# Performance work log

Measured on AMD Instinct MI355X. Metric: run time of the kernel, lower is better.

The kernel has to match this reference:

```python
import jax, jax.numpy as jnp
import numpy as np

SCALES = [2 ** i for i in range(11)]  # init: scales=10 -> [1,2,...,1024]
B, N, C, K = 8, 1024, 256, 4096


def setup_inputs() -> dict:
    key = jax.random.key(0)
    k1, k2, k3 = jax.random.split(key, 3)
    f_BNC = jax.random.normal(k1, (B, N, C), dtype=jnp.float32)
    base = jax.random.normal(k2, (K, C), dtype=jnp.float32)          # orthogonal-init codebook base
    proj_w = jax.random.normal(k3, (C, C), dtype=jnp.float32) / np.float32(np.sqrt(C))  # xavier-ish
    proj_b = jnp.zeros((C,), dtype=jnp.float32)
    return {"f_BNC": f_BNC, "base": base, "proj_w": proj_w, "proj_b": proj_b}


def _linear_interp(x, out_size):
    # x: [B, C, n] -> [B, C, out_size], matches F.interpolate(mode='linear', align_corners=False)
    n = x.shape[-1]
    scale = n / out_size
    src = jnp.maximum((jnp.arange(out_size, dtype=jnp.float32) + 0.5) * scale - 0.5, 0.0)
    i0 = jnp.floor(src).astype(jnp.int32)
    i1 = jnp.minimum(i0 + 1, n - 1)
    w = (src - i0.astype(jnp.float32)).astype(x.dtype)
    return x[..., i0] * (1.0 - w) + x[..., i1] * w


def reference(f_BNC, base, proj_w, proj_b):
    sg = jax.lax.stop_gradient
    # update_embedding(): embedding = proj(base)
    embedding = base @ proj_w.T + proj_b                 # [K, C]
    emb_ng = sg(embedding)
    e_sq = jnp.sum(emb_ng * emb_ng, axis=1)              # [K]

    f_BCN = jnp.transpose(f_BNC, (0, 2, 1))              # [B, C, N]
    f_ng = sg(f_BCN)
    f_rest = f_ng
    f_hat = jnp.zeros_like(f_ng)
    commit = jnp.float32(0.0)
    qlat = jnp.float32(0.0)
    SN = len(SCALES)

    for pn in SCALES:
        # area interpolation == exact mean pooling since N % pn == 0
        rest_BCp = f_rest.reshape(B, C, pn, N // pn).mean(axis=-1)       # [B, C, pn]
        q = jnp.transpose(rest_BCp, (0, 2, 1)).reshape(-1, C)            # [B*pn, C]
        # squared-distance to codebook (gradients never flow through d: argmin only)
        d = jnp.sum(q * q, axis=1, keepdims=True) + e_sq - 2.0 * (q @ emb_ng.T)  # [B*pn, K]
        idx = jnp.argmin(d, axis=1)                                      # [B*pn]
        h_BnC = embedding[idx].reshape(B, pn, C)                         # gather (grad flows to codebook)
        h_BCn = _linear_interp(jnp.transpose(h_BnC, (0, 2, 1)), N)       # [B, C, N]
        f_hat = f_hat + h_BCn
        # residual feeds only argmin at the next scale -> dead gradient path in torch too
        f_rest = f_rest - sg(h_BCn)
        commit = commit + 0.25 * jnp.mean((sg(f_hat) - f_BCN) ** 2)
        qlat = qlat + jnp.mean((f_hat - f_ng) ** 2)

    commit = commit / SN
    qlat = qlat / SN
    # straight-through: f_hat = (f_hat.data - f_no_grad) + f_BCN
    f_out = sg(f_hat) - f_ng + f_BCN
    return (jnp.transpose(f_out, (0, 2, 1)), commit, qlat)
```

## Files before the change

### kernel.cpp

```cpp
#include <hip/hip_runtime.h>
#include <cfloat>

#define BB 8
#define NN 1024
#define CC 256
#define KK 4096
#define SN 11
#define BNC (BB*NN*CC)
#define RMAX 8192

typedef __attribute__((ext_vector_type(8))) _Float16 half8;
typedef __attribute__((ext_vector_type(4))) float f32x4;

__device__ __forceinline__ void split2(float v, ushort& h, ushort& l) {
    union { _Float16 f; ushort u; } a, b;
    a.f = (_Float16)v;
    b.f = (_Float16)(v - (float)a.f);
    h = a.u; l = b.u;
}

__global__ void transpose_pw(const float* __restrict__ pw, float* __restrict__ pwT) {
    int j = blockIdx.x;
    int c = threadIdx.x;
    pwT[j * CC + c] = pw[c * CC + j];
}

__global__ __launch_bounds__(256) void embed_kernel(
    const float* __restrict__ base, const float* __restrict__ pwT,
    const float* __restrict__ pb, float* __restrict__ emb,
    ushort* __restrict__ eh, ushort* __restrict__ el, float* __restrict__ esq) {
    __shared__ float bs[16][CC];
    __shared__ float wpart[16][4];
    int k0 = blockIdx.x * 16;
    int t = threadIdx.x;
    int w = t >> 6, lane = t & 63;
    for (int i = t; i < 16 * CC; i += 256) bs[i >> 8][i & 255] = base[k0 * CC + i];
    __syncthreads();
    float acc[16];
#pragma unroll
    for (int m = 0; m < 16; ++m) acc[m] = 0.f;
    for (int j = 0; j < CC; ++j) {
        float wv = pwT[j * CC + t];
#pragma unroll
        for (int m = 0; m < 16; ++m) acc[m] += bs[m][j] * wv;
    }
    float bias = pb[t];
#pragma unroll
    for (int m = 0; m < 16; ++m) {
        float v = acc[m] + bias;
        int o = (k0 + m) * CC + t;
        emb[o] = v;
        ushort h, l;
        split2(64.f * v, h, l);
        eh[o] = h; el[o] = l;
        float sq = v * v;
#pragma unroll
        for (int d = 1; d < 64; d <<= 1) sq += __shfl_xor(sq, d);
        if (lane == 0) wpart[m][w] = sq;
    }
    __syncthreads();
    if (t < 16) esq[k0 + t] = wpart[t][0] + wpart[t][1] + wpart[t][2] + wpart[t][3];
}

__global__ __launch_bounds__(256) void init_pool16(const float* __restrict__ f,
                                                   float* __restrict__ p16) {
    int blk = blockIdx.x;
    int t = threadIdx.x;
    size_t base = (size_t)blk * 16 * CC + t;
    float s = 0.f;
#pragma unroll
    for (int j = 0; j < 16; ++j) s += f[base + (size_t)j * CC];
    p16[(size_t)blk * CC + t] = s;
}

__global__ void poolB(const float* __restrict__ p16, float* __restrict__ qf, int pnn) {
    int r = blockIdx.x;
    int b = r / pnn, p = r - b * pnn;
    int g16 = 64 / pnn;
    int c4 = threadIdx.x;
    const float4* src = (const float4*)(p16 + ((size_t)b * 64 + (size_t)p * g16) * CC) + c4;
    float4 s = make_float4(0.f, 0.f, 0.f, 0.f);
    for (int i = 0; i < g16; ++i) {
        float4 v = src[(size_t)i * 64];
        s.x += v.x; s.y += v.y; s.z += v.z; s.w += v.w;
    }
    float inv = 1.f / (float)(g16 * 16);
    s.x *= inv; s.y *= inv; s.z *= inv; s.w *= inv;
    ((float4*)(qf + (size_t)r * CC))[c4] = s;
}

__global__ __launch_bounds__(256, 4) void dist_small(
    const float* __restrict__ qf, const float* __restrict__ emb,
    const float* __restrict__ esq, int R,
    float* __restrict__ pval, int* __restrict__ pidx) {
    __shared__ float qs[32][CC];
    __shared__ float es[64][33];
    int t = threadIdx.x;
    int ws = t >> 6, j = t & 63;
    int k0 = blockIdx.x * 64;
    int r0c = blockIdx.y * 32;
    {
        int row = t >> 3, c0 = (t & 7) * 32;
        int gr = r0c + row;
#pragma unroll
        for (int i = 0; i < 8; ++i) {
            float4 v = (gr < R) ? *(const float4*)&qf[(size_t)gr * CC + c0 + 4 * i]
                                : make_float4(0.f, 0.f, 0.f, 0.f);
            *(float4*)&qs[row][c0 + 4 * i] = v;
        }
    }
    float acc[8];
#pragma unroll
    for (int ri = 0; ri < 8; ++ri) acc[ri] = 0.f;
    for (int ck = 0; ck < 8; ++ck) {
        __syncthreads();
        {
            int code = t >> 2, cb = (t & 3) * 8;
            float4 v0 = *(const float4*)&emb[(size_t)(k0 + code) * CC + ck * 32 + cb];
            float4 v1 = *(const float4*)&emb[(size_t)(k0 + code) * CC + ck * 32 + cb + 4];
            es[code][cb + 0] = v0.x; es[code][cb + 1] = v0.y;
            es[code][cb + 2] = v0.z; es[code][cb + 3] = v0.w;
            es[code][cb + 4] = v1.x; es[code][cb + 5] = v1.y;
            es[code][cb + 6] = v1.z; es[code][cb + 7] = v1.w;
        }
        __syncthreads();
        for (int c = 0; c < 32; ++c) {
            float ev = es[j][c];
#pragma unroll
            for (int ri = 0; ri < 8; ++ri)
                acc[ri] += qs[ws + 4 * ri][ck * 32 + c] * ev;
        }
    }
    float esv = esq[k0 + j];
#pragma unroll
    for (int ri = 0; ri < 8; ++ri) {
        int r = r0c + ws + 4 * ri;
        if (r >= R) continue;
        float v = esv - 2.f * acc[ri];
        int bi = k0 + j;
#pragma unroll
        for (int d = 1; d < 64; d <<= 1) {
            float ov = __shfl_xor(v, d);
            int oi = __shfl_xor(bi, d);
            if (ov < v || (ov == v && oi < bi)) { v = ov; bi = oi; }
        }
        if (j == 0) {
            pval[(size_t)r * 64 + blockIdx.x] = v;
            pidx[(size_t)r * 64 + blockIdx.x] = bi;
        }
    }
}

__global__ __launch_bounds__(256, 2) void dist_mfma(
    const ushort* __restrict__ qh, const ushort* __restrict__ ql,
    const ushort* __restrict__ eh, const ushort* __restrict__ el,
    const float* __restrict__ esq,
    float* __restrict__ pval, int* __restrict__ pidx) {
    __shared__ ushort tiles[4096 * 8];
    __shared__ float wv[2][128];
    __shared__ int wi[2][128];
    int t = threadIdx.x;
    int w = t >> 6, lane = t & 63;
    int l15 = lane & 15, hi = lane >> 4;
    int wr = w >> 1, wc = w & 1;
    int r0 = blockIdx.x * 128;
    int kb = blockIdx.y;
    int k0 = kb * 128;

    f32x4 acc[4][4];
#pragma unroll
    for (int mi = 0; mi < 4; ++mi)
#pragma unroll
        for (int ni = 0; ni < 4; ++ni) acc[mi][ni] = (f32x4){0.f, 0.f, 0.f, 0.f};

    for (int ck = 0; ck < 4; ++ck) {
        __syncthreads();
#pragma unroll
        for (int it = 0; it < 16; ++it) {
            int s = it * 256 + t;
            const ushort* g;
            if (s < 2048) {
                int a = s >> 10;
                int rem = s & 1023;
                int row = rem >> 3, sr = rem & 7;
                int c = (ck << 6) + ((sr ^ (row & 7)) << 3);
                g = (a ? ql : qh) + (size_t)(r0 + row) * CC + c;
            } else {
                int s2 = s - 2048;
                int b = s2 >> 10;
                int rem = s2 & 1023;
                int kcol = rem >> 3, sr = rem & 7;
                int c = (ck << 6) + ((sr ^ (kcol & 7)) << 3);
                g = (b ? el : eh) + (size_t)(k0 + kcol) * CC + c;
            }
            ushort* lb = &tiles[(size_t)(it * 256 + (w << 6)) * 8];
            __builtin_amdgcn_global_load_lds(
                (const __attribute__((address_space(1))) unsigned int*)g,
                (__attribute__((address_space(3))) unsigned int*)lb, 16, 0, 0);
        }
        __syncthreads();

#pragma unroll
        for (int kk = 0; kk < 2; ++kk) {
            int cs = (kk << 2) + hi;
            half8 bf0[4], bf1[4], af[4];
#pragma unroll
            for (int ni = 0; ni < 4; ++ni) {
                int kcol = (wc << 6) + (ni << 4) + l15;
                int sb = 2048 + (kcol << 3) + (cs ^ (kcol & 7));
                bf0[ni] = *(const half8*)&tiles[sb * 8];
                bf1[ni] = *(const half8*)&tiles[(sb + 1024) * 8];
            }
#pragma unroll
            for (int mi = 0; mi < 4; ++mi) {
                int row = (wr << 6) + (mi << 4) + l15;
                af[mi] = *(const half8*)&tiles[((row << 3) + (cs ^ (row & 7))) * 8];
            }
#pragma unroll
            for (int mi = 0; mi < 4; ++mi)
#pragma unroll
                for (int ni = 0; ni < 4; ++ni)
                    acc[mi][ni] = __builtin_amdgcn_mfma_f32_16x16x32_f16(af[mi], bf0[ni], acc[mi][ni], 0, 0, 0);
#pragma unroll
            for (int mi = 0; mi < 4; ++mi)
#pragma unroll
                for (int ni = 0; ni < 4; ++ni)
                    acc[mi][ni] = __builtin_amdgcn_mfma_f32_16x16x32_f16(af[mi], bf1[ni], acc[mi][ni], 0, 0, 0);
#pragma unroll
            for (int mi = 0; mi < 4; ++mi) {
                int row = (wr << 6) + (mi << 4) + l15;
                af[mi] = *(const half8*)&tiles[(1024 + (row << 3) + (cs ^ (row & 7))) * 8];
            }
#pragma unroll
            for (int mi = 0; mi < 4; ++mi)
#pragma unroll
                for (int ni = 0; ni < 4; ++ni)
                    acc[mi][ni] = __builtin_amdgcn_mfma_f32_16x16x32_f16(af[mi], bf0[ni], acc[mi][ni], 0, 0, 0);
        }
    }

    int cbase = k0 + (wc << 6) + l15;
    float es4[4];
#pragma unroll
    for (int ni = 0; ni < 4; ++ni) es4[ni] = 4096.f * esq[cbase + ni * 16];
#pragma unroll
    for (int mi = 0; mi < 4; ++mi) {
#pragma unroll
        for (int reg = 0; reg < 4; ++reg) {
            float v = es4[0] - 2.f * acc[mi][0][reg];
            int i = cbase;
#pragma unroll
            for (int ni = 1; ni < 4; ++ni) {
                float v1 = es4[ni] - 2.f * acc[mi][ni][reg];
                if (v1 < v) { v = v1; i = cbase + ni * 16; }
            }
#pragma unroll
            for (int d = 1; d < 16; d <<= 1) {
                float ov = __shfl_xor(v, d);
                int oi = __shfl_xor(i, d);
                if (ov < v || (ov == v && oi < i)) { v = ov; i = oi; }
            }
            if (l15 == 0) {
                int row = (wr << 6) + (mi << 4) + (hi << 2) + reg;
                wv[wc][row] = v;
                wi[wc][row] = i;
            }
        }
    }
    __syncthreads();
    if (t < 128) {
        float v = wv[0][t];
        int i = wi[0][t];
        float ov = wv[1][t];
        int oi = wi[1][t];
        if (ov < v || (ov == v && oi < i)) { v = ov; i = oi; }
        pval[(size_t)(r0 + t) * 64 + kb] = v;
        pidx[(size_t)(r0 + t) * 64 + kb] = i;
    }
}

__global__ __launch_bounds__(256) void update_pool(
    const float* __restrict__ emb, const float* __restrict__ pval,
    const int* __restrict__ pidx, const float* __restrict__ f,
    float* __restrict__ fhat, float* __restrict__ parts,
    ushort* __restrict__ qh, ushort* __restrict__ ql,
    float* __restrict__ qf, float* __restrict__ p16u,
    int pn, int gn, int pnn, int ks) {
    int blk = blockIdx.x;
    int b = blk >> 6, n16 = blk & 63;
    int t = threadIdx.x;
    int w = t >> 6, lane = t & 63;
    int n0 = n16 * 16;
    const float scale = (float)pn * (1.0f / 1024.0f);
    float s_lo = (n0 + 0.5f) * scale - 0.5f;
    if (s_lo < 0.f) s_lo = 0.f;
    int r_lo = (int)s_lo;
    float s_hi = (n0 + 15.5f) * scale - 0.5f;
    if (s_hi < 0.f) s_hi = 0.f;
    int r_hi = min((int)s_hi + 1, pn - 1);
    int cnt = r_hi - r_lo + 1;
    __shared__ int sidx[20];
    for (int ri = w; ri < cnt; ri += 4) {
        size_t rowg = (size_t)(b * pn + r_lo + ri) * 64;
        float v = (lane < ks) ? pval[rowg + lane] : FLT_MAX;
        int i = (lane < ks) ? pidx[rowg + lane] : 0x7fffffff;
#pragma unroll
        for (int d = 1; d < 64; d <<= 1) {
            float ov = __shfl_xor(v, d);
            int oi = __shfl_xor(i, d);
            if (ov < v || (ov == v && oi < i)) { v = ov; i = oi; }
        }
        if (lane == 0) sidx[ri] = i;
    }
    __syncthreads();
    float sq = 0.f;
    float pr = 0.f;
    for (int j = 0; j < 16; ++j) {
        int n = n0 + j;
        float s = (n + 0.5f) * scale - 0.5f;
        if (s < 0.f) s = 0.f;
        int i0 = (int)s;
        float wgt = s - (float)i0;
        int i1 = min(i0 + 1, pn - 1);
        int k0 = sidx[i0 - r_lo];
        int k1 = sidx[i1 - r_lo];
        float e0 = emb[(size_t)k0 * CC + t];
        float e1 = emb[(size_t)k1 * CC + t];
        float h = (1.f - wgt) * e0 + wgt * e1;
        size_t o = ((size_t)b * NN + n) * CC + t;
        float fh = fhat[o] + h;
        fhat[o] = fh;
        float fv = f[o];
        float d = fh - fv;
        sq += d * d;
        pr += (fv - fh);
        if (gn > 0 && gn < 16 && ((j & (gn - 1)) == (gn - 1))) {
            float mean = pr * (1.f / (float)gn);
            ushort H, L;
            split2(64.f * mean, H, L);
            size_t r = (size_t)b * pnn + (size_t)(n / gn);
            qh[r * CC + t] = H;
            ql[r * CC + t] = L;
            pr = 0.f;
        }
    }
    if (gn == 16) qf[(size_t)blk * CC + t] = pr * (1.f / 16.f);
    else if (gn >= 32) p16u[(size_t)blk * CC + t] = pr;
    for (int off = 32; off > 0; off >>= 1) sq += __shfl_down(sq, off);
    __shared__ float wred[4];
    if (lane == 0) wred[w] = sq;
    __syncthreads();
    if (t == 0) parts[blk] = wred[0] + wred[1] + wred[2] + wred[3];
}

__global__ void reduce_final(const float* __restrict__ parts, float* __restrict__ out) {
    __shared__ float red[256];
    int t = threadIdx.x;
    float s = 0.f;
    for (int i = t; i < SN * 512; i += 256) s += parts[i];
    red[t] = s;
    __syncthreads();
    for (int k = 128; k > 0; k >>= 1) {
        if (t < k) red[t] += red[t + k];
        __syncthreads();
    }
    if (t == 0) {
        float mean_sum = red[0] / (float)BNC;
        out[BNC] = 0.25f * mean_sum / (float)SN;
        out[BNC + 1] = mean_sum / (float)SN;
    }
}

extern "C" void kernel_launch(void* const* d_in, const int* in_sizes, int n_in,
                              void* d_out, int out_size, void* d_ws, size_t ws_size,
                              hipStream_t stream) {
    const float* f    = (const float*)d_in[0];
    const float* base = (const float*)d_in[1];
    const float* pw   = (const float*)d_in[2];
    const float* pb   = (const float*)d_in[3];
    float* out = (float*)d_out;

    float* emb   = (float*)d_ws;
    float* esq   = emb + (size_t)KK * CC;
    float* pwT   = esq + KK;
    float* parts = pwT + (size_t)CC * CC;
    float* pval  = parts + (size_t)SN * 512;
    float* p16   = pval + (size_t)RMAX * 64;
    float* p16u  = p16 + (size_t)BB * 64 * CC;
    float* qf    = p16u + (size_t)BB * 64 * CC;
    int*   pidx  = (int*)(qf + (size_t)512 * CC);
    ushort* eh = (ushort*)(pidx + (size_t)RMAX * 64);
    ushort* el = eh + (size_t)KK * CC;
    ushort* qh = el + (size_t)KK * CC;
    ushort* ql = qh + (size_t)RMAX * CC;

    hipMemsetAsync(out, 0, (size_t)BNC * sizeof(float), stream);

    transpose_pw<<<CC, CC, 0, stream>>>(pw, pwT);
    embed_kernel<<<KK / 16, 256, 0, stream>>>(base, pwT, pb, emb, eh, el, esq);
    init_pool16<<<BB * 64, 256, 0, stream>>>(f, p16);
    poolB<<<8, 64, 0, stream>>>(p16, qf, 1);

    for (int sidx = 0; sidx < SN; ++sidx) {
        int pn = 1 << sidx;
        int R = BB * pn;
        int ks;
        if (pn <= 64) {
            dim3 grid(64, (R + 31) / 32);
            dist_small<<<grid, 256, 0, stream>>>(qf, emb, esq, R, pval, pidx);
            ks = 64;
        } else {
            dist_mfma<<<dim3(R / 128, 32), 256, 0, stream>>>(qh, ql, eh, el, esq, pval, pidx);
            ks = 32;
        }
        int pnn = (sidx < SN - 1) ? (pn << 1) : 0;
        int gn = pnn ? (NN / pnn) : 0;
        update_pool<<<BB * 64, 256, 0, stream>>>(emb, pval, pidx, f, out,
                                                 parts + (size_t)sidx * 512,
                                                 qh, ql, qf, p16u, pn, gn, pnn, ks);
        if (pnn && gn >= 32) poolB<<<BB * pnn, 64, 0, stream>>>(p16u, qf, pnn);
    }
    reduce_final<<<1, 256, 0, stream>>>(parts, out);
}
```

Baseline: 560.9 us.

## Track residual instead of f_hat, fuse pooling into dist_small, vectorize update

update_pool now reads and writes the residual (f - f_hat) directly, so each scale does one read and one write instead of reading f_hat and f and writing f_hat. The output is produced only at the final scale as f - residual, which also removes the memset of the output. The separate poolB kernel is dropped and its pooling is folded into dist_small's query load. update_pool switches to float4 accesses and stages rows in LDS for the pooled outputs. This costs an extra full-size residual buffer in workspace and some redundant pooling work across dist_small blocks.

```diff
diff --git a/kernel.cpp b/kernel.cpp
--- a/kernel.cpp
+++ b/kernel.cpp
@@ -66,32 +66,20 @@
                                                    float* __restrict__ p16) {
     int blk = blockIdx.x;
     int t = threadIdx.x;
-    size_t base = (size_t)blk * 16 * CC + t;
-    float s = 0.f;
-#pragma unroll
-    for (int j = 0; j < 16; ++j) s += f[base + (size_t)j * CC];
-    p16[(size_t)blk * CC + t] = s;
-}
-
-__global__ void poolB(const float* __restrict__ p16, float* __restrict__ qf, int pnn) {
-    int r = blockIdx.x;
-    int b = r / pnn, p = r - b * pnn;
-    int g16 = 64 / pnn;
-    int c4 = threadIdx.x;
-    const float4* src = (const float4*)(p16 + ((size_t)b * 64 + (size_t)p * g16) * CC) + c4;
+    int c4 = t & 63;
+    const float4* src = (const float4*)(f + (size_t)blk * 16 * CC) + c4;
     float4 s = make_float4(0.f, 0.f, 0.f, 0.f);
-    for (int i = 0; i < g16; ++i) {
-        float4 v = src[(size_t)i * 64];
+#pragma unroll
+    for (int j = 0; j < 16; ++j) {
+        float4 v = src[(size_t)j * 64];
         s.x += v.x; s.y += v.y; s.z += v.z; s.w += v.w;
     }
-    float inv = 1.f / (float)(g16 * 16);
-    s.x *= inv; s.y *= inv; s.z *= inv; s.w *= inv;
-    ((float4*)(qf + (size_t)r * CC))[c4] = s;
+    ((float4*)(p16 + (size_t)blk * CC))[c4] = s;
 }
 
 __global__ __launch_bounds__(256, 4) void dist_small(
-    const float* __restrict__ qf, const float* __restrict__ emb,
-    const float* __restrict__ esq, int R,
+    const float* __restrict__ src, const float* __restrict__ emb,
+    const float* __restrict__ esq, int R, int g16, int pn, float inv,
     float* __restrict__ pval, int* __restrict__ pidx) {
     __shared__ float qs[32][CC];
     __shared__ float es[64][33];
@@ -100,13 +88,28 @@
     int k0 = blockIdx.x * 64;
     int r0c = blockIdx.y * 32;
     {
-        int row = t >> 3, c0 = (t & 7) * 32;
+        int row = t >> 3;
+        int f4b = (t & 7) * 8;
         int gr = r0c + row;
-#pragma unroll
-        for (int i = 0; i < 8; ++i) {
-            float4 v = (gr < R) ? *(const float4*)&qf[(size_t)gr * CC + c0 + 4 * i]
-                                : make_float4(0.f, 0.f, 0.f, 0.f);
-            *(float4*)&qs[row][c0 + 4 * i] = v;
+        float4 a4[8];
+#pragma unroll
+        for (int ii = 0; ii < 8; ++ii) a4[ii] = make_float4(0.f, 0.f, 0.f, 0.f);
+        if (gr < R) {
+            int b = gr / pn, p = gr - b * pn;
+            const float4* sp = (const float4*)(src + ((size_t)b * 64 + (size_t)p * g16) * CC) + f4b;
+            for (int i = 0; i < g16; ++i) {
+#pragma unroll
+                for (int ii = 0; ii < 8; ++ii) {
+                    float4 v = sp[ii];
+                    a4[ii].x += v.x; a4[ii].y += v.y; a4[ii].z += v.z; a4[ii].w += v.w;
+                }
+                sp += 64;
+            }
+        }
+#pragma unroll
+        for (int ii = 0; ii < 8; ++ii) {
+            a4[ii].x *= inv; a4[ii].y *= inv; a4[ii].z *= inv; a4[ii].w *= inv;
+            *(float4*)&qs[row][(f4b + ii) * 4] = a4[ii];
         }
     }
     float acc[8];
@@ -281,11 +284,12 @@
 
 __global__ __launch_bounds__(256) void update_pool(
     const float* __restrict__ emb, const float* __restrict__ pval,
-    const int* __restrict__ pidx, const float* __restrict__ f,
-    float* __restrict__ fhat, float* __restrict__ parts,
+    const int* __restrict__ pidx, const float* __restrict__ rin,
+    float* __restrict__ rout, const float* __restrict__ f,
+    float* __restrict__ outp, float* __restrict__ parts,
     ushort* __restrict__ qh, ushort* __restrict__ ql,
     float* __restrict__ qf, float* __restrict__ p16u,
-    int pn, int gn, int pnn, int ks) {
+    int pn, int gn, int pnn, int ks, int finalflag) {
     int blk = blockIdx.x;
     int b = blk >> 6, n16 = blk & 63;
     int t = threadIdx.x;
@@ -313,9 +317,14 @@
         if (lane == 0) sidx[ri] = i;
     }
     __syncthreads();
+    __shared__ float4 rlds[16][64];
+    __shared__ float wred[4];
+    int nsub = t >> 6;
+    int c4 = t & 63;
     float sq = 0.f;
-    float pr = 0.f;
-    for (int j = 0; j < 16; ++j) {
+#pragma unroll
+    for (int jj = 0; jj < 4; ++jj) {
+        int j = nsub + 4 * jj;
         int n = n0 + j;
         float s = (n + 0.5f) * scale - 0.5f;
         if (s < 0.f) s = 0.f;
@@ -324,33 +333,50 @@
         int i1 = min(i0 + 1, pn - 1);
         int k0 = sidx[i0 - r_lo];
         int k1 = sidx[i1 - r_lo];
-        float e0 = emb[(size_t)k0 * CC + t];
-        float e1 = emb[(size_t)k1 * CC + t];
-        float h = (1.f - wgt) * e0 + wgt * e1;
-        size_t o = ((size_t)b * NN + n) * CC + t;
-        float fh = fhat[o] + h;
-        fhat[o] = fh;
-        float fv = f[o];
-        float d = fh - fv;
-        sq += d * d;
-        pr += (fv - fh);
-        if (gn > 0 && gn < 16 && ((j & (gn - 1)) == (gn - 1))) {
-            float mean = pr * (1.f / (float)gn);
-            ushort H, L;
-            split2(64.f * mean, H, L);
-            size_t r = (size_t)b * pnn + (size_t)(n / gn);
-            qh[r * CC + t] = H;
-            ql[r * CC + t] = L;
-            pr = 0.f;
-        }
-    }
-    if (gn == 16) qf[(size_t)blk * CC + t] = pr * (1.f / 16.f);
-    else if (gn >= 32) p16u[(size_t)blk * CC + t] = pr;
+        float4 e0 = ((const float4*)(emb + (size_t)k0 * CC))[c4];
+        float4 e1 = ((const float4*)(emb + (size_t)k1 * CC))[c4];
+        float wm = 1.f - wgt;
+        float4 h = make_float4(wm * e0.x + wgt * e1.x, wm * e0.y + wgt * e1.y,
+                               wm * e0.z + wgt * e1.z, wm * e0.w + wgt * e1.w);
+        size_t o4 = ((size_t)b * NN + n) * 64 + c4;
+        float4 rv0 = ((const float4*)rin)[o4];
+        float4 rv = make_float4(rv0.x - h.x, rv0.y - h.y, rv0.z - h.z, rv0.w - h.w);
+        if (!finalflag) {
+            ((float4*)rout)[o4] = rv;
+        } else {
+            float4 fv = ((const float4*)f)[o4];
+            ((float4*)outp)[o4] = make_float4(fv.x - rv.x, fv.y - rv.y,
+                                              fv.z - rv.z, fv.w - rv.w);
+        }
+        sq += rv.x * rv.x + rv.y * rv.y + rv.z * rv.z + rv.w * rv.w;
+        rlds[j][c4] = rv;
+    }
     for (int off = 32; off > 0; off >>= 1) sq += __shfl_down(sq, off);
-    __shared__ float wred[4];
     if (lane == 0) wred[w] = sq;
     __syncthreads();
     if (t == 0) parts[blk] = wred[0] + wred[1] + wred[2] + wred[3];
+    if (gn == 0) return;
+    const float* rl = (const float*)rlds;
+    if (gn < 16) {
+        float pr = 0.f;
+        for (int j = 0; j < 16; ++j) {
+            pr += rl[j * CC + t];
+            if ((j & (gn - 1)) == (gn - 1)) {
+                float mean = pr * (1.f / (float)gn);
+                ushort H, L;
+                split2(64.f * mean, H, L);
+                size_t r = (size_t)b * pnn + (size_t)((n0 + j) / gn);
+                qh[r * CC + t] = H;
+                ql[r * CC + t] = L;
+                pr = 0.f;
+            }
+        }
+    } else {
+        float pr = 0.f;
+        for (int j = 0; j < 16; ++j) pr += rl[j * CC + t];
+        if (gn == 16) qf[(size_t)blk * CC + t] = pr * (1.f / 16.f);
+        else p16u[(size_t)blk * CC + t] = pr;
+    }
 }
 
 __global__ void reduce_final(const float* __restrict__ parts, float* __restrict__ out) {
@@ -388,26 +414,30 @@
     float* p16   = pval + (size_t)RMAX * 64;
     float* p16u  = p16 + (size_t)BB * 64 * CC;
     float* qf    = p16u + (size_t)BB * 64 * CC;
-    int*   pidx  = (int*)(qf + (size_t)512 * CC);
+    float* resid = qf + (size_t)512 * CC;
+    int*   pidx  = (int*)(resid + BNC);
     ushort* eh = (ushort*)(pidx + (size_t)RMAX * 64);
     ushort* el = eh + (size_t)KK * CC;
     ushort* qh = el + (size_t)KK * CC;
     ushort* ql = qh + (size_t)RMAX * CC;
 
-    hipMemsetAsync(out, 0, (size_t)BNC * sizeof(float), stream);
-
     transpose_pw<<<CC, CC, 0, stream>>>(pw, pwT);
     embed_kernel<<<KK / 16, 256, 0, stream>>>(base, pwT, pb, emb, eh, el, esq);
     init_pool16<<<BB * 64, 256, 0, stream>>>(f, p16);
-    poolB<<<8, 64, 0, stream>>>(p16, qf, 1);
 
     for (int sidx = 0; sidx < SN; ++sidx) {
         int pn = 1 << sidx;
         int R = BB * pn;
         int ks;
         if (pn <= 64) {
+            const float* src;
+            float inv;
+            int g16;
+            if (pn == 64)      { src = qf;   g16 = 1;       inv = 1.f; }
+            else if (pn == 1)  { src = p16;  g16 = 64;      inv = 1.f / 1024.f; }
+            else               { src = p16u; g16 = 64 / pn; inv = 1.f / (16.f * (64 / pn)); }
             dim3 grid(64, (R + 31) / 32);
-            dist_small<<<grid, 256, 0, stream>>>(qf, emb, esq, R, pval, pidx);
+            dist_small<<<grid, 256, 0, stream>>>(src, emb, esq, R, g16, pn, inv, pval, pidx);
             ks = 64;
         } else {
             dist_mfma<<<dim3(R / 128, 32), 256, 0, stream>>>(qh, ql, eh, el, esq, pval, pidx);
@@ -415,10 +445,11 @@
         }
         int pnn = (sidx < SN - 1) ? (pn << 1) : 0;
         int gn = pnn ? (NN / pnn) : 0;
-        update_pool<<<BB * 64, 256, 0, stream>>>(emb, pval, pidx, f, out,
+        const float* rin = (sidx == 0) ? f : resid;
+        update_pool<<<BB * 64, 256, 0, stream>>>(emb, pval, pidx, rin, resid, f, out,
                                                  parts + (size_t)sidx * 512,
-                                                 qh, ql, qf, p16u, pn, gn, pnn, ks);
-        if (pnn && gn >= 32) poolB<<<BB * pnn, 64, 0, stream>>>(p16u, qf, pnn);
+                                                 qh, ql, qf, p16u, pn, gn, pnn, ks,
+                                                 (sidx == SN - 1) ? 1 : 0);
     }
     reduce_final<<<1, 256, 0, stream>>>(parts, out);
 }
```

Result: no change. 560.3 us (-0.1%).
